# Kernel tuning notes

Hardware: AMD Instinct MI355X
Metric: run time of the kernel (lower is better)

Reference implementation:

```python
import jax, jax.numpy as jnp
import numpy as np

B, H, W = 16, 1024, 1024


def setup_inputs() -> dict:
    key = jax.random.key(0)
    k1, k2, k3 = jax.random.split(key, 3)
    predicted_images = jax.random.normal(k1, (B, H, W, 2), dtype=jnp.float32)
    char_gt = jax.random.uniform(k2, (B, H, W), dtype=jnp.float32)
    aff_gt = jax.random.uniform(k3, (B, H, W), dtype=jnp.float32)
    return {"predicted_images": predicted_images, "char_gt": char_gt, "aff_gt": aff_gt}


def reference(predicted_images, char_gt, aff_gt):
    # Faithful to the torch code: after view([B*H*W, 1]) each "image" in
    # forward_once is a single pixel (num_all = 1), so sum_positive <= 1,
    # k = min(3*sum_positive, 1 - sum_positive) < 10 always, and avg_loss
    # is mse_loss.mean() for every pixel. Mean over the B*H*W per-pixel
    # losses == global mean squared error per channel; total = char + aff.
    pred_char = predicted_images[..., 0]  # [B,H,W]
    pred_aff = predicted_images[..., 1]   # [B,H,W]
    loss_char = jnp.mean(jnp.square(pred_char - char_gt))
    loss_aff = jnp.mean(jnp.square(pred_aff - aff_gt))
    return loss_char + loss_aff
```

## Files before the change

kernel.cpp:

```cpp
#include <hip/hip_runtime.h>

#define NPIX (16u * 1024u * 1024u)
#define NQUADS (NPIX / 4u)
#define NBLOCKS 2048
#define NTHREADS 256

__global__ __launch_bounds__(NTHREADS) void ohem_partial_kernel(
    const float4* __restrict__ pred4,
    const float4* __restrict__ cgt4,
    const float4* __restrict__ agt4,
    float* __restrict__ partials) {
  const unsigned tid = blockIdx.x * NTHREADS + threadIdx.x;
  const unsigned stride = gridDim.x * NTHREADS;

  float acc = 0.0f;
  for (unsigned q = tid; q < NQUADS; q += stride) {
    float4 p01 = pred4[2u * q];
    float4 p23 = pred4[2u * q + 1u];
    float4 c = cgt4[q];
    float4 a = agt4[q];
    float d;
    d = p01.x - c.x; acc = fmaf(d, d, acc);
    d = p01.z - c.y; acc = fmaf(d, d, acc);
    d = p23.x - c.z; acc = fmaf(d, d, acc);
    d = p23.z - c.w; acc = fmaf(d, d, acc);
    d = p01.y - a.x; acc = fmaf(d, d, acc);
    d = p01.w - a.y; acc = fmaf(d, d, acc);
    d = p23.y - a.z; acc = fmaf(d, d, acc);
    d = p23.w - a.w; acc = fmaf(d, d, acc);
  }

  #pragma unroll
  for (int off = 32; off > 0; off >>= 1) acc += __shfl_down(acc, off, 64);

  __shared__ float smem[NTHREADS / 64];
  const int wave = threadIdx.x >> 6;
  if ((threadIdx.x & 63) == 0) smem[wave] = acc;
  __syncthreads();
  if (threadIdx.x == 0) {
    float t = 0.0f;
    #pragma unroll
    for (int w = 0; w < NTHREADS / 64; ++w) t += smem[w];
    partials[blockIdx.x] = t;
  }
}

__global__ __launch_bounds__(NTHREADS) void ohem_final_kernel(
    const float* __restrict__ partials, float* __restrict__ out) {
  double acc = 0.0;
  for (int i = threadIdx.x; i < NBLOCKS; i += NTHREADS) acc += (double)partials[i];

  #pragma unroll
  for (int off = 32; off > 0; off >>= 1) acc += __shfl_down(acc, off, 64);

  __shared__ double smem[NTHREADS / 64];
  const int wave = threadIdx.x >> 6;
  if ((threadIdx.x & 63) == 0) smem[wave] = acc;
  __syncthreads();
  if (threadIdx.x == 0) {
    double t = 0.0;
    #pragma unroll
    for (int w = 0; w < NTHREADS / 64; ++w) t += smem[w];
    out[0] = (float)(t / (double)NPIX);
  }
}

extern "C" void kernel_launch(void* const* d_in, const int* in_sizes, int n_in,
                              void* d_out, int out_size, void* d_ws, size_t ws_size,
                              hipStream_t stream) {
  const float4* pred4 = (const float4*)d_in[0];
  const float4* cgt4 = (const float4*)d_in[1];
  const float4* agt4 = (const float4*)d_in[2];
  float* out = (float*)d_out;
  float* partials = (float*)d_ws;

  ohem_partial_kernel<<<NBLOCKS, NTHREADS, 0, stream>>>(pred4, cgt4, agt4, partials);
  ohem_final_kernel<<<1, NTHREADS, 0, stream>>>(partials, out);
}
```

Measured before the change: 47.20 us.

## Fuse final reduction into main kernel via last-block atomic counter

Replaces the separate single-block finalize kernel with a last-block-done pattern: each block publishes its partial with release semantics and bumps an atomic ticket, and the final block sums all partials in double. The main loop now handles eight pixels per thread per iteration with a compile-time trip count and unroll of two, for more loads in flight. This removes one kernel launch and its dependency gap but adds a memset launch to reset the counter, plus atomic traffic.

```diff
diff --git a/kernel.cpp b/kernel.cpp
--- a/kernel.cpp
+++ b/kernel.cpp
@@ -1,67 +1,94 @@
 #include <hip/hip_runtime.h>
 
 #define NPIX (16u * 1024u * 1024u)
-#define NQUADS (NPIX / 4u)
+#define NOCTS (NPIX / 8u)
 #define NBLOCKS 2048
 #define NTHREADS 256
+#define NITERS (NOCTS / (NBLOCKS * NTHREADS))
 
-__global__ __launch_bounds__(NTHREADS) void ohem_partial_kernel(
+#define PARTIALS_OFF 256
+
+__global__ __launch_bounds__(NTHREADS) void ohem_fused_kernel(
     const float4* __restrict__ pred4,
     const float4* __restrict__ cgt4,
     const float4* __restrict__ agt4,
-    float* __restrict__ partials) {
+    unsigned* __restrict__ counter,
+    float* __restrict__ partials,
+    float* __restrict__ out) {
   const unsigned tid = blockIdx.x * NTHREADS + threadIdx.x;
-  const unsigned stride = gridDim.x * NTHREADS;
+  const unsigned stride = NBLOCKS * NTHREADS;
 
   float acc = 0.0f;
-  for (unsigned q = tid; q < NQUADS; q += stride) {
-    float4 p01 = pred4[2u * q];
-    float4 p23 = pred4[2u * q + 1u];
-    float4 c = cgt4[q];
-    float4 a = agt4[q];
+  #pragma unroll 2
+  for (unsigned it = 0; it < NITERS; ++it) {
+    const unsigned o = tid + it * stride;
+    const float4 p0 = pred4[4u * o + 0u];
+    const float4 p1 = pred4[4u * o + 1u];
+    const float4 p2 = pred4[4u * o + 2u];
+    const float4 p3 = pred4[4u * o + 3u];
+    const float4 c0 = cgt4[2u * o + 0u];
+    const float4 c1 = cgt4[2u * o + 1u];
+    const float4 a0 = agt4[2u * o + 0u];
+    const float4 a1 = agt4[2u * o + 1u];
     float d;
-    d = p01.x - c.x; acc = fmaf(d, d, acc);
-    d = p01.z - c.y; acc = fmaf(d, d, acc);
-    d = p23.x - c.z; acc = fmaf(d, d, acc);
-    d = p23.z - c.w; acc = fmaf(d, d, acc);
-    d = p01.y - a.x; acc = fmaf(d, d, acc);
-    d = p01.w - a.y; acc = fmaf(d, d, acc);
-    d = p23.y - a.z; acc = fmaf(d, d, acc);
-    d = p23.w - a.w; acc = fmaf(d, d, acc);
+    d = p0.x - c0.x; acc = fmaf(d, d, acc);
+    d = p0.z - c0.y; acc = fmaf(d, d, acc);
+    d = p1.x - c0.z; acc = fmaf(d, d, acc);
+    d = p1.z - c0.w; acc = fmaf(d, d, acc);
+    d = p2.x - c1.x; acc = fmaf(d, d, acc);
+    d = p2.z - c1.y; acc = fmaf(d, d, acc);
+    d = p3.x - c1.z; acc = fmaf(d, d, acc);
+    d = p3.z - c1.w; acc = fmaf(d, d, acc);
+    d = p0.y - a0.x; acc = fmaf(d, d, acc);
+    d = p0.w - a0.y; acc = fmaf(d, d, acc);
+    d = p1.y - a0.z; acc = fmaf(d, d, acc);
+    d = p1.w - a0.w; acc = fmaf(d, d, acc);
+    d = p2.y - a1.x; acc = fmaf(d, d, acc);
+    d = p2.w - a1.y; acc = fmaf(d, d, acc);
+    d = p3.y - a1.z; acc = fmaf(d, d, acc);
+    d = p3.w - a1.w; acc = fmaf(d, d, acc);
   }
 
   #pragma unroll
   for (int off = 32; off > 0; off >>= 1) acc += __shfl_down(acc, off, 64);
 
-  __shared__ float smem[NTHREADS / 64];
+  __shared__ float smemf[NTHREADS / 64];
+  __shared__ bool is_last;
   const int wave = threadIdx.x >> 6;
-  if ((threadIdx.x & 63) == 0) smem[wave] = acc;
+  if ((threadIdx.x & 63) == 0) smemf[wave] = acc;
   __syncthreads();
+
   if (threadIdx.x == 0) {
     float t = 0.0f;
     #pragma unroll
-    for (int w = 0; w < NTHREADS / 64; ++w) t += smem[w];
-    partials[blockIdx.x] = t;
+    for (int w = 0; w < NTHREADS / 64; ++w) t += smemf[w];
+    __hip_atomic_store(&partials[blockIdx.x], t, __ATOMIC_RELEASE,
+                       __HIP_MEMORY_SCOPE_AGENT);
+    unsigned ticket = __hip_atomic_fetch_add(counter, 1u, __ATOMIC_ACQ_REL,
+                                             __HIP_MEMORY_SCOPE_AGENT);
+    is_last = (ticket == NBLOCKS - 1u);
   }
-}
+  __syncthreads();
 
-__global__ __launch_bounds__(NTHREADS) void ohem_final_kernel(
-    const float* __restrict__ partials, float* __restrict__ out) {
-  double acc = 0.0;
-  for (int i = threadIdx.x; i < NBLOCKS; i += NTHREADS) acc += (double)partials[i];
+  if (is_last) {
+    double dacc = 0.0;
+    for (int i = threadIdx.x; i < NBLOCKS; i += NTHREADS) {
+      float v = __hip_atomic_load(&partials[i], __ATOMIC_RELAXED,
+                                  __HIP_MEMORY_SCOPE_AGENT);
+      dacc += (double)v;
+    }
+    #pragma unroll
+    for (int off = 32; off > 0; off >>= 1) dacc += __shfl_down(dacc, off, 64);
 
-  #pragma unroll
-  for (int off = 32; off > 0; off >>= 1) acc += __shfl_down(acc, off, 64);
-
-  __shared__ double smem[NTHREADS / 64];
-  const int wave = threadIdx.x >> 6;
-  if ((threadIdx.x & 63) == 0) smem[wave] = acc;
-  __syncthreads();
-  if (threadIdx.x == 0) {
-    double t = 0.0;
-    #pragma unroll
-    for (int w = 0; w < NTHREADS / 64; ++w) t += smem[w];
-    out[0] = (float)(t / (double)NPIX);
+    __shared__ double smemd[NTHREADS / 64];
+    if ((threadIdx.x & 63) == 0) smemd[wave] = dacc;
+    __syncthreads();
+    if (threadIdx.x == 0) {
+      double t = 0.0;
+      #pragma unroll
+      for (int w = 0; w < NTHREADS / 64; ++w) t += smemd[w];
+      out[0] = (float)(t / (double)NPIX);
+    }
   }
 }
 
@@ -72,8 +99,10 @@
   const float4* cgt4 = (const float4*)d_in[1];
   const float4* agt4 = (const float4*)d_in[2];
   float* out = (float*)d_out;
-  float* partials = (float*)d_ws;
+  unsigned* counter = (unsigned*)d_ws;
+  float* partials = (float*)((char*)d_ws + PARTIALS_OFF);
 
-  ohem_partial_kernel<<<NBLOCKS, NTHREADS, 0, stream>>>(pred4, cgt4, agt4, partials);
-  ohem_final_kernel<<<1, NTHREADS, 0, stream>>>(partials, out);
+  hipMemsetAsync(counter, 0, sizeof(unsigned), stream);
+  ohem_fused_kernel<<<NBLOCKS, NTHREADS, 0, stream>>>(pred4, cgt4, agt4,
+                                                      counter, partials, out);
 }
```

Measured after the change: 163.9 us. 247% more time.
